# Kernel optimization log

Hardware: AMD Instinct MI355X
Metric: run time of the kernel (lower is better)

## Reference

```python
import jax, jax.numpy as jnp
import numpy as np
import math

H, DK, G_DIM, S_DIM, HID = 8, 64, 512, 3072, 512
B = 16384
EPS = 1e-5

def _layernorm(x, g, b):
    mu = jnp.mean(x, axis=-1, keepdims=True)
    var = jnp.mean((x - mu) ** 2, axis=-1, keepdims=True)
    return (x - mu) * jax.lax.rsqrt(var + EPS) * g + b

def setup_inputs() -> dict:
    key = jax.random.key(0)
    ks = jax.random.split(key, 12)
    s = 0.02
    return {
        "h_g": jax.random.normal(ks[0], (B, G_DIM), jnp.float32),
        "h_s": jax.random.normal(ks[1], (B, S_DIM), jnp.float32),
        # stacked per-head projections: [H, in_dim, d_k]
        "Wq": jax.random.normal(ks[2], (H, G_DIM, DK), jnp.float32) * s,
        "bq": jnp.zeros((H, DK), jnp.float32),
        "Wk": jax.random.normal(ks[3], (H, S_DIM, DK), jnp.float32) * s,
        "bk": jnp.zeros((H, DK), jnp.float32),
        "Wv": jax.random.normal(ks[4], (H, S_DIM, DK), jnp.float32) * s,
        "bv": jnp.zeros((H, DK), jnp.float32),
        "Wo": jax.random.normal(ks[5], (HID, HID), jnp.float32) * s,
        "bo": jnp.zeros((HID,), jnp.float32),
        "ln1_g": jnp.ones((HID,), jnp.float32),
        "ln1_b": jnp.zeros((HID,), jnp.float32),
        "W1": jax.random.normal(ks[6], (HID, 2 * HID), jnp.float32) * s,
        "b1": jnp.zeros((2 * HID,), jnp.float32),
        "W2": jax.random.normal(ks[7], (2 * HID, HID), jnp.float32) * s,
        "b2": jnp.zeros((HID,), jnp.float32),
        "ln2_g": jnp.ones((HID,), jnp.float32),
        "ln2_b": jnp.zeros((HID,), jnp.float32),
    }

def reference(h_g, h_s, Wq, bq, Wk, bk, Wv, bv, Wo, bo, ln1_g, ln1_b, W1, b1, W2, b2, ln2_g, ln2_b):
    b = h_g.shape[0]
    # batched per-head projections (fuses the per-head Linear loop)
    Q = jnp.einsum('bg,hgd->bhd', h_g, Wq) + bq          # [B,H,DK]
    K = jnp.einsum('bs,hsd->bhd', h_s, Wk) + bk          # [B,H,DK]
    V = jnp.einsum('bs,hsd->bhd', h_s, Wv) + bv          # [B,H,DK]
    # seq_len == 1: scores is [B,H,1]; softmax over a single key == 1
    scores = jnp.sum(Q * K, axis=-1, keepdims=True) / math.sqrt(DK)
    attn_w = jax.nn.softmax(scores, axis=-1)             # identically ones
    attn = attn_w * V                                    # == V
    h_concat = attn.reshape(b, H * DK)                   # [B,HID]
    h_attn = h_concat @ Wo + bo
    h_attn = _layernorm(h_attn + h_g, ln1_g, ln1_b)
    # MLP (dropout is identity in eval mode); torch GELU default = exact erf
    h = jax.nn.gelu(h_attn @ W1 + b1, approximate=False) @ W2 + b2
    return _layernorm(h + h_attn, ln2_g, ln2_b)
```

## Files before the change

kernel.cpp:

```cpp
#include <hip/hip_runtime.h>
#include <hip/hip_bf16.h>
#include <math.h>

#define HH    8
#define DKK   64
#define GD    512
#define SD    3072
#define HID_  512
#define BB    16384

typedef unsigned short ushort_t;
typedef __attribute__((ext_vector_type(8))) short bf16x8;
typedef __attribute__((ext_vector_type(4))) float f32x4;

__device__ __forceinline__ float bf2f(ushort_t u) {
  union { unsigned int i; float f; } c; c.i = ((unsigned int)u) << 16; return c.f;
}
__device__ __forceinline__ ushort_t f2bf(float f) {
  union { float f; unsigned int i; } c; c.f = f;
  unsigned int x = c.i;
  return (ushort_t)((x + 0x7FFFu + ((x >> 16) & 1u)) >> 16);
}
__device__ __forceinline__ unsigned int pk_bf16(float a, float b) {
  __hip_bfloat162 h = __float22bfloat162_rn(make_float2(a, b));
  union { __hip_bfloat162 h; unsigned int u; } c; c.h = h; return c.u;
}

__device__ __forceinline__ void async_cp16(const ushort_t* gsrc, ushort_t* ldst) {
  __builtin_amdgcn_global_load_lds(
      (const __attribute__((address_space(1))) unsigned int*)gsrc,
      (__attribute__((address_space(3))) unsigned int*)ldst, 16, 0, 0);
}

__device__ __forceinline__ float gelu_tanh(float x) {
  float y = 0.79788456080286535588f * (x + 0.044715f * x * x * x);
  float e = __expf(2.0f * y);
  float th = 1.0f - 2.0f / (e + 1.0f);
  return 0.5f * x * (1.0f + th);
}

template <int EPI>
__global__ __launch_bounds__(256) void gemm_bt(
    const ushort_t* __restrict__ A, const ushort_t* __restrict__ Bt,
    ushort_t* __restrict__ C, const float* __restrict__ bias,
    int M, int N, int K) {
  __shared__ __align__(16) ushort_t As[128 * 32];
  __shared__ __align__(16) ushort_t Bs[128 * 32];
  const int tid = threadIdx.x;
  const int wv = tid >> 6;
  const int lane = tid & 63;
  const int m0 = blockIdx.y * 128;
  const int n0 = blockIdx.x * 128;
  const int srow = lane >> 2;
  const int scol = (lane & 3) * 8;
  const int wm = wv & 1, wn = wv >> 1;
  const int lr = lane & 15, quad = lane >> 4;

  f32x4 acc[4][4];
#pragma unroll
  for (int i = 0; i < 4; ++i)
#pragma unroll
    for (int j = 0; j < 4; ++j) acc[i][j] = (f32x4){0.f, 0.f, 0.f, 0.f};

  const ushort_t* Ab = A + (size_t)m0 * K;
  const ushort_t* Bb = Bt + (size_t)n0 * K;

  for (int k0 = 0; k0 < K; k0 += 32) {
    __syncthreads();
#pragma unroll
    for (int i = 0; i < 2; ++i) {
      const int chunk = i * 4 + wv;
      const int row = chunk * 16 + srow;
      async_cp16(Ab + (size_t)row * K + (k0 + scol), As + chunk * 512);
      async_cp16(Bb + (size_t)row * K + (k0 + scol), Bs + chunk * 512);
    }
    __syncthreads();
    bf16x8 af[4], bfr[4];
#pragma unroll
    for (int i = 0; i < 4; ++i)
      af[i] = *(const bf16x8*)&As[(wm * 64 + i * 16 + lr) * 32 + quad * 8];
#pragma unroll
    for (int j = 0; j < 4; ++j)
      bfr[j] = *(const bf16x8*)&Bs[(wn * 64 + j * 16 + lr) * 32 + quad * 8];
#pragma unroll
    for (int i = 0; i < 4; ++i)
#pragma unroll
      for (int j = 0; j < 4; ++j)
        acc[i][j] = __builtin_amdgcn_mfma_f32_16x16x32_bf16(af[i], bfr[j], acc[i][j], 0, 0, 0);
  }

#pragma unroll
  for (int i = 0; i < 4; ++i) {
    const int mg = m0 + wm * 64 + i * 16 + quad * 4;
#pragma unroll
    for (int j = 0; j < 4; ++j) {
      const int ng = n0 + wn * 64 + j * 16 + lr;
      const float bvv = bias ? bias[ng] : 0.0f;
#pragma unroll
      for (int r = 0; r < 4; ++r) {
        float v = acc[i][j][r] + bvv;
        if (EPI == 1) v = gelu_tanh(v);
        C[(size_t)(mg + r) * N + ng] = f2bf(v);
      }
    }
  }
}

__global__ __launch_bounds__(256) void gemm_bt_f32a(
    const float* __restrict__ A, const ushort_t* __restrict__ Bt,
    ushort_t* __restrict__ C, const float* __restrict__ bias,
    int M, int N, int K) {
  __shared__ __align__(16) ushort_t As[128 * 32];
  __shared__ __align__(16) ushort_t Bs[128 * 32];
  const int tid = threadIdx.x;
  const int wv = tid >> 6;
  const int lane = tid & 63;
  const int m0 = blockIdx.y * 128;
  const int n0 = blockIdx.x * 128;
  const int srow = lane >> 2;
  const int scol = (lane & 3) * 8;
  const int wm = wv & 1, wn = wv >> 1;
  const int lr = lane & 15, quad = lane >> 4;
  const int arow = tid >> 1;
  const int ach = (tid & 1) * 16;

  f32x4 acc[4][4];
#pragma unroll
  for (int i = 0; i < 4; ++i)
#pragma unroll
    for (int j = 0; j < 4; ++j) acc[i][j] = (f32x4){0.f, 0.f, 0.f, 0.f};

  const float* Ag = A + (size_t)(m0 + arow) * K + ach;
  const ushort_t* Bb = Bt + (size_t)n0 * K;

  for (int k0 = 0; k0 < K; k0 += 32) {
    __syncthreads();
    float4 f0 = *(const float4*)(Ag + k0);
    float4 f1 = *(const float4*)(Ag + k0 + 4);
    float4 f2 = *(const float4*)(Ag + k0 + 8);
    float4 f3 = *(const float4*)(Ag + k0 + 12);
#pragma unroll
    for (int i = 0; i < 2; ++i) {
      const int chunk = i * 4 + wv;
      const int row = chunk * 16 + srow;
      async_cp16(Bb + (size_t)row * K + (k0 + scol), Bs + chunk * 512);
    }
    unsigned int p[8];
    p[0] = pk_bf16(f0.x, f0.y); p[1] = pk_bf16(f0.z, f0.w);
    p[2] = pk_bf16(f1.x, f1.y); p[3] = pk_bf16(f1.z, f1.w);
    p[4] = pk_bf16(f2.x, f2.y); p[5] = pk_bf16(f2.z, f2.w);
    p[6] = pk_bf16(f3.x, f3.y); p[7] = pk_bf16(f3.z, f3.w);
    *(uint4*)&As[arow * 32 + ach] = *(const uint4*)&p[0];
    *(uint4*)&As[arow * 32 + ach + 8] = *(const uint4*)&p[4];
    __syncthreads();
    bf16x8 af[4], bfr[4];
#pragma unroll
    for (int i = 0; i < 4; ++i)
      af[i] = *(const bf16x8*)&As[(wm * 64 + i * 16 + lr) * 32 + quad * 8];
#pragma unroll
    for (int j = 0; j < 4; ++j)
      bfr[j] = *(const bf16x8*)&Bs[(wn * 64 + j * 16 + lr) * 32 + quad * 8];
#pragma unroll
    for (int i = 0; i < 4; ++i)
#pragma unroll
      for (int j = 0; j < 4; ++j)
        acc[i][j] = __builtin_amdgcn_mfma_f32_16x16x32_bf16(af[i], bfr[j], acc[i][j], 0, 0, 0);
  }

#pragma unroll
  for (int i = 0; i < 4; ++i) {
    const int mg = m0 + wm * 64 + i * 16 + quad * 4;
#pragma unroll
    for (int j = 0; j < 4; ++j) {
      const int ng = n0 + wn * 64 + j * 16 + lr;
      const float bvv = bias[ng];
#pragma unroll
      for (int r = 0; r < 4; ++r)
        C[(size_t)(mg + r) * N + ng] = f2bf(acc[i][j][r] + bvv);
    }
  }
}

__global__ __launch_bounds__(256) void permute_wv(const float* __restrict__ Wv,
                                                  ushort_t* __restrict__ Wvp) {
  const int idx = (blockIdx.x * 256 + threadIdx.x) * 8;
  const int s = idx >> 9;
  const int c = idx & 511;
  const float* src = Wv + (size_t)(c >> 6) * (SD * DKK) + (size_t)s * DKK + (c & 63);
  float4 a = *(const float4*)src;
  float4 b = *(const float4*)(src + 4);
  unsigned int p[4];
  p[0] = pk_bf16(a.x, a.y); p[1] = pk_bf16(a.z, a.w);
  p[2] = pk_bf16(b.x, b.y); p[3] = pk_bf16(b.z, b.w);
  *(uint4*)(Wvp + idx) = *(const uint4*)p;
}

__global__ __launch_bounds__(256) void transpose3(
    const float* __restrict__ s0, ushort_t* __restrict__ d0,
    const float* __restrict__ s1, ushort_t* __restrict__ d1,
    const float* __restrict__ s2, ushort_t* __restrict__ d2) {
  __shared__ ushort_t tile[32][33];
  const int z = blockIdx.z;
  const float* src = (z == 0) ? s0 : (z == 1) ? s1 : s2;
  ushort_t* dst = (z == 0) ? d0 : (z == 1) ? d1 : d2;
  const int R = (z == 2) ? 1024 : 512;
  const int C = (z == 1) ? 1024 : 512;
  const int bx = blockIdx.x * 32;
  const int by = blockIdx.y * 32;
  if (bx >= C || by >= R) return;
  const int tx = threadIdx.x, ty = threadIdx.y;
#pragma unroll
  for (int i = 0; i < 32; i += 8)
    tile[ty + i][tx] = f2bf(src[(size_t)(by + ty + i) * C + (bx + tx)]);
  __syncthreads();
#pragma unroll
  for (int i = 0; i < 32; i += 8)
    dst[(size_t)(bx + ty + i) * R + (by + tx)] = tile[tx][ty + i];
}

__global__ __launch_bounds__(256) void c0_kernel(const float* __restrict__ bv,
                                                 const float* __restrict__ Wo,
                                                 const float* __restrict__ bo,
                                                 float* __restrict__ c0) {
  __shared__ float red[8][32];
  const int jl = threadIdx.x & 31;
  const int chunk = threadIdx.x >> 5;
  const int j = blockIdx.x * 32 + jl;
  const int cbase = chunk * 64;
  float s = 0.f;
#pragma unroll 8
  for (int c = 0; c < 64; ++c) s += bv[cbase + c] * Wo[(size_t)(cbase + c) * 512 + j];
  red[chunk][jl] = s;
  __syncthreads();
  if (chunk == 0) {
    float t = bo[j];
#pragma unroll
    for (int q = 0; q < 8; ++q) t += red[q][jl];
    c0[j] = t;
  }
}

template <int RES_F32, int OUT_F32>
__global__ __launch_bounds__(256) void ln_kernel(const ushort_t* __restrict__ t,
                                                 const void* __restrict__ res_,
                                                 const float* __restrict__ g,
                                                 const float* __restrict__ b,
                                                 void* __restrict__ out_) {
  const int row = blockIdx.x * 4 + (threadIdx.x >> 6);
  const int lane = threadIdx.x & 63;
  const size_t base = (size_t)row * 512 + lane * 8;
  uint4 tv = *(const uint4*)(t + base);
  const ushort_t* tp = (const ushort_t*)&tv;
  float r[8];
  if (RES_F32) {
    const float* res = (const float*)res_;
    float4 a = *(const float4*)(res + base);
    float4 c = *(const float4*)(res + base + 4);
    r[0] = a.x; r[1] = a.y; r[2] = a.z; r[3] = a.w;
    r[4] = c.x; r[5] = c.y; r[6] = c.z; r[7] = c.w;
  } else {
    const ushort_t* res = (const ushort_t*)res_;
    uint4 rv = *(const uint4*)(res + base);
    const ushort_t* rp = (const ushort_t*)&rv;
#pragma unroll
    for (int k = 0; k < 8; ++k) r[k] = bf2f(rp[k]);
  }
  float x[8];
  float s = 0.f, sq = 0.f;
#pragma unroll
  for (int k = 0; k < 8; ++k) {
    float v = bf2f(tp[k]) + r[k];
    x[k] = v; s += v; sq += v * v;
  }
#pragma unroll
  for (int off = 32; off > 0; off >>= 1) {
    s += __shfl_xor(s, off);
    sq += __shfl_xor(sq, off);
  }
  const float mean = s * (1.0f / 512.0f);
  const float var = sq * (1.0f / 512.0f) - mean * mean;
  const float rstd = rsqrtf(var + 1e-5f);
  float4 gv0 = *(const float4*)(g + lane * 8);
  float4 gv1 = *(const float4*)(g + lane * 8 + 4);
  float4 bv0 = *(const float4*)(b + lane * 8);
  float4 bv1 = *(const float4*)(b + lane * 8 + 4);
  const float gg[8] = {gv0.x, gv0.y, gv0.z, gv0.w, gv1.x, gv1.y, gv1.z, gv1.w};
  const float bb[8] = {bv0.x, bv0.y, bv0.z, bv0.w, bv1.x, bv1.y, bv1.z, bv1.w};
  float y[8];
#pragma unroll
  for (int k = 0; k < 8; ++k) y[k] = (x[k] - mean) * rstd * gg[k] + bb[k];
  if (OUT_F32) {
    float* out = (float*)out_;
    *(float4*)(out + base) = make_float4(y[0], y[1], y[2], y[3]);
    *(float4*)(out + base + 4) = make_float4(y[4], y[5], y[6], y[7]);
  } else {
    ushort_t* out = (ushort_t*)out_;
    uint4 ov; ushort_t* op = (ushort_t*)&ov;
#pragma unroll
    for (int k = 0; k < 8; ++k) op[k] = f2bf(y[k]);
    *(uint4*)(out + base) = ov;
  }
}

extern "C" void kernel_launch(void* const* d_in, const int* in_sizes, int n_in,
                              void* d_out, int out_size, void* d_ws, size_t ws_size,
                              hipStream_t stream) {
  const float* h_g  = (const float*)d_in[0];
  const float* h_s  = (const float*)d_in[1];
  const float* Wv   = (const float*)d_in[6];
  const float* bv   = (const float*)d_in[7];
  const float* Wo   = (const float*)d_in[8];
  const float* bo   = (const float*)d_in[9];
  const float* ln1g = (const float*)d_in[10];
  const float* ln1b = (const float*)d_in[11];
  const float* W1   = (const float*)d_in[12];
  const float* b1   = (const float*)d_in[13];
  const float* W2   = (const float*)d_in[14];
  const float* b2   = (const float*)d_in[15];
  const float* ln2g = (const float*)d_in[16];
  const float* ln2b = (const float*)d_in[17];

  char* ws = (char*)d_ws;
  ushort_t* WoT = (ushort_t*)(ws + 0);
  ushort_t* W1T = (ushort_t*)(ws + 524288);
  ushort_t* W2T = (ushort_t*)(ws + 1572864);
  ushort_t* Wvp = (ushort_t*)(ws + 2621440);
  ushort_t* WcT = (ushort_t*)(ws + 5767168);
  float*    c0f = (float*)(ws + 8912896);
  ushort_t* t1  = (ushort_t*)(ws + 9437184);
  ushort_t* t2  = t1;
  ushort_t* x   = (ushort_t*)(ws + 26214400);
  ushort_t* u   = (ushort_t*)(ws + 42991616);
  (void)in_sizes; (void)n_in; (void)out_size; (void)ws_size;

  hipLaunchKernelGGL(permute_wv, dim3(768), dim3(256), 0, stream, Wv, Wvp);
  hipLaunchKernelGGL(transpose3, dim3(32, 32, 3), dim3(32, 8), 0, stream,
                     Wo, WoT, W1, W1T, W2, W2T);
  hipLaunchKernelGGL(c0_kernel, dim3(16), dim3(256), 0, stream, bv, Wo, bo, c0f);

  hipLaunchKernelGGL(gemm_bt<0>, dim3(24, 4), dim3(256), 0, stream,
                     WoT, Wvp, WcT, (const float*)nullptr, 512, 3072, 512);
  hipLaunchKernelGGL(gemm_bt_f32a, dim3(4, 128), dim3(256), 0, stream,
                     h_s, WcT, t1, c0f, BB, 512, 3072);
  hipLaunchKernelGGL((ln_kernel<1, 0>), dim3(4096), dim3(256), 0, stream,
                     t1, (const void*)h_g, ln1g, ln1b, (void*)x);
  hipLaunchKernelGGL(gemm_bt<1>, dim3(8, 128), dim3(256), 0, stream,
                     x, W1T, u, b1, BB, 1024, 512);
  hipLaunchKernelGGL(gemm_bt<0>, dim3(4, 128), dim3(256), 0, stream,
                     u, W2T, t2, b2, BB, 512, 1024);
  hipLaunchKernelGGL((ln_kernel<0, 1>), dim3(4096), dim3(256), 0, stream,
                     t2, (const void*)x, ln2g, ln2b, d_out);
}
```

Measured before the change: 574.2 us.

## Split-K the big GEMMs with fp32 partials, XCD-aware block swizzle, async fp32 A loads

The h_s GEMM and the W2 GEMM now use split-K by 2. Each half writes fp32 partial sums, and the following LayerNorm kernels add the two partials plus the bias. A block-index swizzle groups tiles per XCD to improve L2 locality. The fp32 A operand of the h_s GEMM is now brought in with async global_load_lds into a swizzled fp32 LDS tile and converted to bf16 on the LDS read, rather than through register loads. In exchange, the fp32 partials add extra global memory traffic and use more LDS per block.

```diff
diff --git a/kernel.cpp b/kernel.cpp
--- a/kernel.cpp
+++ b/kernel.cpp
@@ -31,6 +31,11 @@
       (const __attribute__((address_space(1))) unsigned int*)gsrc,
       (__attribute__((address_space(3))) unsigned int*)ldst, 16, 0, 0);
 }
+__device__ __forceinline__ void async_cp16f(const float* gsrc, float* ldst) {
+  __builtin_amdgcn_global_load_lds(
+      (const __attribute__((address_space(1))) unsigned int*)gsrc,
+      (__attribute__((address_space(3))) unsigned int*)ldst, 16, 0, 0);
+}
 
 __device__ __forceinline__ float gelu_tanh(float x) {
   float y = 0.79788456080286535588f * (x + 0.044715f * x * x * x);
@@ -39,18 +44,32 @@
   return 0.5f * x * (1.0f + th);
 }
 
-template <int EPI>
+__device__ __forceinline__ void swz_coords(int& nb, int& mb, int& kz) {
+  int NB = gridDim.x, MB = gridDim.y;
+  int bid = blockIdx.x + NB * (blockIdx.y + MB * blockIdx.z);
+  int xcd = bid & 7;
+  int j = bid >> 3;
+  nb = j & (NB - 1);
+  int rest = j / NB;
+  int mk = (rest << 3) | xcd;
+  mb = mk & (MB - 1);
+  kz = mk / MB;
+}
+
+template <int EPI, int SWZ>
 __global__ __launch_bounds__(256) void gemm_bt(
     const ushort_t* __restrict__ A, const ushort_t* __restrict__ Bt,
-    ushort_t* __restrict__ C, const float* __restrict__ bias,
-    int M, int N, int K) {
+    void* __restrict__ Cv, const float* __restrict__ bias,
+    int M, int N, int Kfull, int Klen) {
   __shared__ __align__(16) ushort_t As[128 * 32];
   __shared__ __align__(16) ushort_t Bs[128 * 32];
   const int tid = threadIdx.x;
   const int wv = tid >> 6;
   const int lane = tid & 63;
-  const int m0 = blockIdx.y * 128;
-  const int n0 = blockIdx.x * 128;
+  int nb, mb, kz;
+  if (SWZ) swz_coords(nb, mb, kz);
+  else { nb = blockIdx.x; mb = blockIdx.y; kz = blockIdx.z; }
+  const int m0 = mb * 128, n0 = nb * 128, kbeg = kz * Klen;
   const int srow = lane >> 2;
   const int scol = (lane & 3) * 8;
   const int wm = wv & 1, wn = wv >> 1;
@@ -62,17 +81,17 @@
 #pragma unroll
     for (int j = 0; j < 4; ++j) acc[i][j] = (f32x4){0.f, 0.f, 0.f, 0.f};
 
-  const ushort_t* Ab = A + (size_t)m0 * K;
-  const ushort_t* Bb = Bt + (size_t)n0 * K;
-
-  for (int k0 = 0; k0 < K; k0 += 32) {
+  const ushort_t* Ab = A + (size_t)m0 * Kfull + kbeg;
+  const ushort_t* Bb = Bt + (size_t)n0 * Kfull + kbeg;
+
+  for (int k0 = 0; k0 < Klen; k0 += 32) {
     __syncthreads();
 #pragma unroll
     for (int i = 0; i < 2; ++i) {
       const int chunk = i * 4 + wv;
       const int row = chunk * 16 + srow;
-      async_cp16(Ab + (size_t)row * K + (k0 + scol), As + chunk * 512);
-      async_cp16(Bb + (size_t)row * K + (k0 + scol), Bs + chunk * 512);
+      async_cp16(Ab + (size_t)row * Kfull + (k0 + scol), As + chunk * 512);
+      async_cp16(Bb + (size_t)row * Kfull + (k0 + scol), Bs + chunk * 512);
     }
     __syncthreads();
     bf16x8 af[4], bfr[4];
@@ -95,34 +114,42 @@
 #pragma unroll
     for (int j = 0; j < 4; ++j) {
       const int ng = n0 + wn * 64 + j * 16 + lr;
-      const float bvv = bias ? bias[ng] : 0.0f;
-#pragma unroll
-      for (int r = 0; r < 4; ++r) {
-        float v = acc[i][j][r] + bvv;
-        if (EPI == 1) v = gelu_tanh(v);
-        C[(size_t)(mg + r) * N + ng] = f2bf(v);
+      if (EPI == 2) {
+        float* C = (float*)Cv + (size_t)kz * M * N;
+#pragma unroll
+        for (int r = 0; r < 4; ++r)
+          C[(size_t)(mg + r) * N + ng] = acc[i][j][r];
+      } else {
+        ushort_t* C = (ushort_t*)Cv;
+        const float bvv = bias ? bias[ng] : 0.0f;
+#pragma unroll
+        for (int r = 0; r < 4; ++r) {
+          float v = acc[i][j][r] + bvv;
+          if (EPI == 1) v = gelu_tanh(v);
+          C[(size_t)(mg + r) * N + ng] = f2bf(v);
+        }
       }
     }
   }
 }
 
-__global__ __launch_bounds__(256) void gemm_bt_f32a(
+__global__ __launch_bounds__(256, 4) void gemm_a32(
     const float* __restrict__ A, const ushort_t* __restrict__ Bt,
-    ushort_t* __restrict__ C, const float* __restrict__ bias,
-    int M, int N, int K) {
-  __shared__ __align__(16) ushort_t As[128 * 32];
+    float* __restrict__ C, int M, int N, int Kfull, int Klen) {
+  __shared__ __align__(16) float As4[128 * 32];
   __shared__ __align__(16) ushort_t Bs[128 * 32];
   const int tid = threadIdx.x;
   const int wv = tid >> 6;
   const int lane = tid & 63;
-  const int m0 = blockIdx.y * 128;
-  const int n0 = blockIdx.x * 128;
+  int nb, mb, kz;
+  swz_coords(nb, mb, kz);
+  const int m0 = mb * 128, n0 = nb * 128, kbeg = kz * Klen;
   const int srow = lane >> 2;
   const int scol = (lane & 3) * 8;
   const int wm = wv & 1, wn = wv >> 1;
   const int lr = lane & 15, quad = lane >> 4;
-  const int arow = tid >> 1;
-  const int ach = (tid & 1) * 16;
+  const int a_rc = lane >> 3;
+  const int a_g = (lane & 7) ^ a_rc;
 
   f32x4 acc[4][4];
 #pragma unroll
@@ -130,33 +157,37 @@
 #pragma unroll
     for (int j = 0; j < 4; ++j) acc[i][j] = (f32x4){0.f, 0.f, 0.f, 0.f};
 
-  const float* Ag = A + (size_t)(m0 + arow) * K + ach;
-  const ushort_t* Bb = Bt + (size_t)n0 * K;
-
-  for (int k0 = 0; k0 < K; k0 += 32) {
+  const float* Ab = A + (size_t)m0 * Kfull + kbeg;
+  const ushort_t* Bb = Bt + (size_t)n0 * Kfull + kbeg;
+
+  for (int k0 = 0; k0 < Klen; k0 += 32) {
     __syncthreads();
-    float4 f0 = *(const float4*)(Ag + k0);
-    float4 f1 = *(const float4*)(Ag + k0 + 4);
-    float4 f2 = *(const float4*)(Ag + k0 + 8);
-    float4 f3 = *(const float4*)(Ag + k0 + 12);
 #pragma unroll
     for (int i = 0; i < 2; ++i) {
       const int chunk = i * 4 + wv;
       const int row = chunk * 16 + srow;
-      async_cp16(Bb + (size_t)row * K + (k0 + scol), Bs + chunk * 512);
-    }
-    unsigned int p[8];
-    p[0] = pk_bf16(f0.x, f0.y); p[1] = pk_bf16(f0.z, f0.w);
-    p[2] = pk_bf16(f1.x, f1.y); p[3] = pk_bf16(f1.z, f1.w);
-    p[4] = pk_bf16(f2.x, f2.y); p[5] = pk_bf16(f2.z, f2.w);
-    p[6] = pk_bf16(f3.x, f3.y); p[7] = pk_bf16(f3.z, f3.w);
-    *(uint4*)&As[arow * 32 + ach] = *(const uint4*)&p[0];
-    *(uint4*)&As[arow * 32 + ach + 8] = *(const uint4*)&p[4];
+      async_cp16(Bb + (size_t)row * Kfull + (k0 + scol), Bs + chunk * 512);
+    }
+#pragma unroll
+    for (int t = 0; t < 4; ++t) {
+      const int chunkA = t * 4 + wv;
+      const int r = chunkA * 8 + a_rc;
+      async_cp16f(Ab + (size_t)r * Kfull + (k0 + 4 * a_g), As4 + chunkA * 256);
+    }
     __syncthreads();
     bf16x8 af[4], bfr[4];
 #pragma unroll
-    for (int i = 0; i < 4; ++i)
-      af[i] = *(const bf16x8*)&As[(wm * 64 + i * 16 + lr) * 32 + quad * 8];
+    for (int i = 0; i < 4; ++i) {
+      const int r = wm * 64 + i * 16 + lr;
+      const int x0 = (2 * quad) ^ (lr & 7);
+      const int x1 = (2 * quad + 1) ^ (lr & 7);
+      float4 fa = *(const float4*)&As4[r * 32 + x0 * 4];
+      float4 fb = *(const float4*)&As4[r * 32 + x1 * 4];
+      union { unsigned int u[4]; bf16x8 v; } c;
+      c.u[0] = pk_bf16(fa.x, fa.y); c.u[1] = pk_bf16(fa.z, fa.w);
+      c.u[2] = pk_bf16(fb.x, fb.y); c.u[3] = pk_bf16(fb.z, fb.w);
+      af[i] = c.v;
+    }
 #pragma unroll
     for (int j = 0; j < 4; ++j)
       bfr[j] = *(const bf16x8*)&Bs[(wn * 64 + j * 16 + lr) * 32 + quad * 8];
@@ -167,16 +198,16 @@
         acc[i][j] = __builtin_amdgcn_mfma_f32_16x16x32_bf16(af[i], bfr[j], acc[i][j], 0, 0, 0);
   }
 
+  float* Cp = C + (size_t)kz * M * N;
 #pragma unroll
   for (int i = 0; i < 4; ++i) {
     const int mg = m0 + wm * 64 + i * 16 + quad * 4;
 #pragma unroll
     for (int j = 0; j < 4; ++j) {
       const int ng = n0 + wn * 64 + j * 16 + lr;
-      const float bvv = bias[ng];
 #pragma unroll
       for (int r = 0; r < 4; ++r)
-        C[(size_t)(mg + r) * N + ng] = f2bf(acc[i][j][r] + bvv);
+        Cp[(size_t)(mg + r) * N + ng] = acc[i][j][r];
     }
   }
 }
@@ -241,23 +272,35 @@
 }
 
 template <int RES_F32, int OUT_F32>
-__global__ __launch_bounds__(256) void ln_kernel(const ushort_t* __restrict__ t,
-                                                 const void* __restrict__ res_,
-                                                 const float* __restrict__ g,
-                                                 const float* __restrict__ b,
-                                                 void* __restrict__ out_) {
+__global__ __launch_bounds__(256) void ln_fused(const float* __restrict__ p0,
+                                                const float* __restrict__ p1,
+                                                const float* __restrict__ cb,
+                                                const void* __restrict__ res_,
+                                                const float* __restrict__ g,
+                                                const float* __restrict__ b,
+                                                void* __restrict__ out_) {
   const int row = blockIdx.x * 4 + (threadIdx.x >> 6);
   const int lane = threadIdx.x & 63;
   const size_t base = (size_t)row * 512 + lane * 8;
-  uint4 tv = *(const uint4*)(t + base);
-  const ushort_t* tp = (const ushort_t*)&tv;
+  const int col = lane * 8;
+  float4 a0 = *(const float4*)(p0 + base);
+  float4 a1 = *(const float4*)(p0 + base + 4);
+  float4 c0v = *(const float4*)(p1 + base);
+  float4 c1v = *(const float4*)(p1 + base + 4);
+  float4 d0 = *(const float4*)(cb + col);
+  float4 d1 = *(const float4*)(cb + col + 4);
+  float t[8];
+  t[0] = a0.x + c0v.x + d0.x; t[1] = a0.y + c0v.y + d0.y;
+  t[2] = a0.z + c0v.z + d0.z; t[3] = a0.w + c0v.w + d0.w;
+  t[4] = a1.x + c1v.x + d1.x; t[5] = a1.y + c1v.y + d1.y;
+  t[6] = a1.z + c1v.z + d1.z; t[7] = a1.w + c1v.w + d1.w;
   float r[8];
   if (RES_F32) {
     const float* res = (const float*)res_;
-    float4 a = *(const float4*)(res + base);
-    float4 c = *(const float4*)(res + base + 4);
-    r[0] = a.x; r[1] = a.y; r[2] = a.z; r[3] = a.w;
-    r[4] = c.x; r[5] = c.y; r[6] = c.z; r[7] = c.w;
+    float4 e0 = *(const float4*)(res + base);
+    float4 e1 = *(const float4*)(res + base + 4);
+    r[0] = e0.x; r[1] = e0.y; r[2] = e0.z; r[3] = e0.w;
+    r[4] = e1.x; r[5] = e1.y; r[6] = e1.z; r[7] = e1.w;
   } else {
     const ushort_t* res = (const ushort_t*)res_;
     uint4 rv = *(const uint4*)(res + base);
@@ -269,7 +312,7 @@
   float s = 0.f, sq = 0.f;
 #pragma unroll
   for (int k = 0; k < 8; ++k) {
-    float v = bf2f(tp[k]) + r[k];
+    float v = t[k] + r[k];
     x[k] = v; s += v; sq += v * v;
   }
 #pragma unroll
@@ -280,10 +323,10 @@
   const float mean = s * (1.0f / 512.0f);
   const float var = sq * (1.0f / 512.0f) - mean * mean;
   const float rstd = rsqrtf(var + 1e-5f);
-  float4 gv0 = *(const float4*)(g + lane * 8);
-  float4 gv1 = *(const float4*)(g + lane * 8 + 4);
-  float4 bv0 = *(const float4*)(b + lane * 8);
-  float4 bv1 = *(const float4*)(b + lane * 8 + 4);
+  float4 gv0 = *(const float4*)(g + col);
+  float4 gv1 = *(const float4*)(g + col + 4);
+  float4 bv0 = *(const float4*)(b + col);
+  float4 bv1 = *(const float4*)(b + col + 4);
   const float gg[8] = {gv0.x, gv0.y, gv0.z, gv0.w, gv1.x, gv1.y, gv1.z, gv1.w};
   const float bb[8] = {bv0.x, bv0.y, bv0.z, bv0.w, bv1.x, bv1.y, bv1.z, bv1.w};
   float y[8];
@@ -327,10 +370,12 @@
   ushort_t* Wvp = (ushort_t*)(ws + 2621440);
   ushort_t* WcT = (ushort_t*)(ws + 5767168);
   float*    c0f = (float*)(ws + 8912896);
-  ushort_t* t1  = (ushort_t*)(ws + 9437184);
-  ushort_t* t2  = t1;
-  ushort_t* x   = (ushort_t*)(ws + 26214400);
-  ushort_t* u   = (ushort_t*)(ws + 42991616);
+  float*    p0  = (float*)(ws + 16777216);
+  float*    p1  = (float*)(ws + 50331648);
+  ushort_t* x   = (ushort_t*)(ws + 83886080);
+  ushort_t* u   = (ushort_t*)(ws + 100663296);
+  float*    q0  = p0;
+  float*    q1  = p1;
   (void)in_sizes; (void)n_in; (void)out_size; (void)ws_size;
 
   hipLaunchKernelGGL(permute_wv, dim3(768), dim3(256), 0, stream, Wv, Wvp);
@@ -338,16 +383,16 @@
                      Wo, WoT, W1, W1T, W2, W2T);
   hipLaunchKernelGGL(c0_kernel, dim3(16), dim3(256), 0, stream, bv, Wo, bo, c0f);
 
-  hipLaunchKernelGGL(gemm_bt<0>, dim3(24, 4), dim3(256), 0, stream,
-                     WoT, Wvp, WcT, (const float*)nullptr, 512, 3072, 512);
-  hipLaunchKernelGGL(gemm_bt_f32a, dim3(4, 128), dim3(256), 0, stream,
-                     h_s, WcT, t1, c0f, BB, 512, 3072);
-  hipLaunchKernelGGL((ln_kernel<1, 0>), dim3(4096), dim3(256), 0, stream,
-                     t1, (const void*)h_g, ln1g, ln1b, (void*)x);
-  hipLaunchKernelGGL(gemm_bt<1>, dim3(8, 128), dim3(256), 0, stream,
-                     x, W1T, u, b1, BB, 1024, 512);
-  hipLaunchKernelGGL(gemm_bt<0>, dim3(4, 128), dim3(256), 0, stream,
-                     u, W2T, t2, b2, BB, 512, 1024);
-  hipLaunchKernelGGL((ln_kernel<0, 1>), dim3(4096), dim3(256), 0, stream,
-                     t2, (const void*)x, ln2g, ln2b, d_out);
-}
+  hipLaunchKernelGGL((gemm_bt<0, 0>), dim3(24, 4, 1), dim3(256), 0, stream,
+                     WoT, Wvp, (void*)WcT, (const float*)nullptr, 512, 3072, 512, 512);
+  hipLaunchKernelGGL(gemm_a32, dim3(4, 128, 2), dim3(256), 0, stream,
+                     h_s, WcT, p0, BB, 512, 3072, 1536);
+  hipLaunchKernelGGL((ln_fused<1, 0>), dim3(4096), dim3(256), 0, stream,
+                     p0, p1, c0f, (const void*)h_g, ln1g, ln1b, (void*)x);
+  hipLaunchKernelGGL((gemm_bt<1, 1>), dim3(8, 128, 1), dim3(256), 0, stream,
+                     x, W1T, (void*)u, b1, BB, 1024, 512, 512);
+  hipLaunchKernelGGL((gemm_bt<2, 1>), dim3(4, 128, 2), dim3(256), 0, stream,
+                     u, W2T, (void*)q0, (const float*)nullptr, BB, 512, 1024, 512);
+  hipLaunchKernelGGL((ln_fused<0, 1>), dim3(4096), dim3(256), 0, stream,
+                     q0, q1, b2, (const void*)x, ln2g, ln2b, d_out);
+}
```

After: 550.2 us. 1.04x faster.
